# Performance work log

Measured on AMD Instinct MI355X. Metric: run time of the kernel, lower is better.

## Reference

```python
import jax, jax.numpy as jnp
import numpy as np

GROUPS = 32
EPS = 1e-6


def group_norm(x, gamma, beta):
    b, h, w, c = x.shape
    xg = x.reshape(b, h, w, GROUPS, c // GROUPS)
    mean = jnp.mean(xg, axis=(1, 2, 4), keepdims=True)
    var = jnp.var(xg, axis=(1, 2, 4), keepdims=True)
    xg = (xg - mean) * jax.lax.rsqrt(var + EPS)
    return xg.reshape(b, h, w, c) * gamma + beta


def setup_inputs() -> dict:
    key = jax.random.key(0)
    ks = jax.random.split(key, 6)
    B, H, W, C = 4, 64, 64, 512
    scale = 0.02
    return {
        "x": jax.random.normal(ks[0], (B, H, W, C), dtype=jnp.float32),
        "gamma": jnp.ones((C,), dtype=jnp.float32),
        "beta": jnp.zeros((C,), dtype=jnp.float32),
        "wq": jax.random.normal(ks[1], (C, C), dtype=jnp.float32) * scale,
        "bq": jnp.zeros((C,), dtype=jnp.float32),
        "wk": jax.random.normal(ks[2], (C, C), dtype=jnp.float32) * scale,
        "bk": jnp.zeros((C,), dtype=jnp.float32),
        "wv": jax.random.normal(ks[3], (C, C), dtype=jnp.float32) * scale,
        "bv": jnp.zeros((C,), dtype=jnp.float32),
        "wo": jax.random.normal(ks[4], (C, C), dtype=jnp.float32) * scale,
        "bo": jnp.zeros((C,), dtype=jnp.float32),
    }


def reference(x, gamma, beta, wq, bq, wk, bk, wv, bv, wo, bo):
    b, h, w, c = x.shape
    xn = group_norm(x, gamma, beta)
    # 1x1 convs == per-pixel linear layers
    q = (jnp.einsum('bhwc,cd->bhwd', xn, wq) + bq).reshape(b, h * w, c)
    k = (jnp.einsum('bhwc,cd->bhwd', xn, wk) + bk).reshape(b, h * w, c)
    v = (jnp.einsum('bhwc,cd->bhwd', xn, wv) + bv).reshape(b, h * w, c)
    # full (hw x hw) attention, single head
    scores = jnp.einsum('bic,bjc->bij', q, k) * (c ** -0.5)  # [b, hw, hw]
    attn = jax.nn.softmax(scores, axis=-1)
    out = jnp.einsum('bij,bjc->bic', attn, v).reshape(b, h, w, c)
    return jnp.einsum('bhwc,cd->bhwd', out, wo) + bo + x
```

## Files before the change

### kernel.cpp

```cpp
#include <hip/hip_runtime.h>
#include <stdint.h>


typedef __attribute__((ext_vector_type(8))) short bf16x8;
typedef __attribute__((ext_vector_type(8))) unsigned short u16x8;
typedef __attribute__((ext_vector_type(4))) float f32x4;

#define SOFTMAX_SCALE 0.044194173824159216f
#define QSCALE 0.06376237087058025f

__device__ __forceinline__ unsigned short f2bf(float f) {
  unsigned int x = __float_as_uint(f);
  x += 0x7fffu + ((x >> 16) & 1u);
  return (unsigned short)(x >> 16);
}
__device__ __forceinline__ float bf2f(unsigned short u) {
  return __uint_as_float((unsigned int)u << 16);
}

__device__ __forceinline__ void gl_lds16(const void* g, void* l) {
  __builtin_amdgcn_global_load_lds(
      (__attribute__((address_space(1))) unsigned char*)g,
      (__attribute__((address_space(3))) unsigned char*)l, 16, 0, 0);
}

__device__ __forceinline__ void gemm_tile(
    const unsigned short* __restrict__ A, long lda,
    const unsigned short* __restrict__ B, long ldb,
    int K, unsigned short* As, unsigned short* Bs, f32x4 acc[4][4]) {
  const int tid = threadIdx.x;
  const int wave = tid >> 6, lane = tid & 63;
  const int srow = lane >> 3;
  const int gg = lane & 7;
  const int wm = (wave >> 1) * 64, wn = (wave & 1) * 64;
  const int lrow = lane & 15;
  const int rsw = lrow & 7;
  const int kgb = lane >> 4;

  for (int k0 = 0; k0 < K; k0 += 64) {
    __syncthreads();
    for (int i = 0; i < 4; ++i) {
      int chunk = wave * 4 + i;
      int row = chunk * 8 + srow;
      int soffA = (gg ^ srow) * 16;
      int soffB = (gg ^ ((chunk * 2 + (srow >> 2)) & 7)) * 16;
      gl_lds16((const char*)(A + (long)row * lda + k0) + soffA, (char*)As + chunk * 1024);
      gl_lds16((const char*)(B + (long)row * ldb + k0) + soffB, (char*)Bs + chunk * 1024);
    }
    __syncthreads();
#pragma unroll
    for (int ks = 0; ks < 2; ++ks) {
      bf16x8 af[4], bfr[4];
      const int off = ((ks * 4 + kgb) ^ rsw) * 8;
#pragma unroll
      for (int t = 0; t < 4; ++t) {
        af[t]  = *(const bf16x8*)&As[(wm + t * 16 + lrow) * 64 + off];
        bfr[t] = *(const bf16x8*)&Bs[(wn + 4 * lrow + t) * 64 + off];
      }
#pragma unroll
      for (int mt = 0; mt < 4; ++mt)
#pragma unroll
        for (int nt = 0; nt < 4; ++nt)
          acc[mt][nt] = __builtin_amdgcn_mfma_f32_16x16x32_bf16(af[mt], bfr[nt], acc[mt][nt], 0, 0, 0);
    }
  }
}

#define EPILOG_SETUP                                          \
  const int lane = threadIdx.x & 63, wave = threadIdx.x >> 6; \
  const int wm = (wave >> 1) * 64, wn = (wave & 1) * 64;      \
  const int lcol4 = (lane & 15) * 4, lrb = (lane >> 4) * 4;

__global__ void prep_kernel(const float* __restrict__ wq, const float* __restrict__ wk,
                            const float* __restrict__ wv, const float* __restrict__ wo,
                            const float* __restrict__ bq, const float* __restrict__ bk,
                            const float* __restrict__ bv,
                            unsigned short* __restrict__ wqkvT,
                            unsigned short* __restrict__ woT,
                            float* __restrict__ bias, float* __restrict__ stats,
                            float* __restrict__ lsum) {
  long id = (long)blockIdx.x * 256 + threadIdx.x;
  if (id < 786432) {
    long n = id >> 9, k = id & 511;
    const float* w = (n < 512) ? wq : (n < 1024 ? wk : wv);
    wqkvT[id] = f2bf(w[k * 512 + (n & 511)]);
  } else if (id < 786432 + 262144) {
    long j = id - 786432, n = j >> 9, k = j & 511;
    woT[j] = f2bf(wo[k * 512 + n]);
  } else if (id < 786432 + 262144 + 1536) {
    long j = id - 786432 - 262144;
    bias[j] = (j < 512) ? bq[j] : (j < 1024 ? bk[j - 512] : bv[j - 1024]);
  } else if (id < 786432 + 262144 + 1536 + 256) {
    stats[id - 786432 - 262144 - 1536] = 0.f;
  } else if (id < 786432 + 262144 + 1536 + 256 + 16384) {
    lsum[id - 786432 - 262144 - 1536 - 256] = 0.f;
  }
}

__global__ __launch_bounds__(256) void gn_stats(const float* __restrict__ x,
                                                float* __restrict__ stats) {
  const int b = blockIdx.x >> 7, slab = blockIdx.x & 127;
  const float* xp = x + (long)b * 4096 * 512 + (long)slab * 32 * 512;
  const int tid = threadIdx.x;
  float s = 0.f, s2 = 0.f;
  for (int it = 0; it < 16; ++it) {
    int i = it * 256 + tid;
    float4 v = *(const float4*)(xp + (long)i * 4);
    s += v.x + v.y + v.z + v.w;
    s2 += v.x * v.x + v.y * v.y + v.z * v.z + v.w * v.w;
  }
  s += __shfl_xor(s, 1); s += __shfl_xor(s, 2);
  s2 += __shfl_xor(s2, 1); s2 += __shfl_xor(s2, 2);
  if ((tid & 3) == 0) {
    int g = (tid & 127) >> 2;
    atomicAdd(&stats[(b * 32 + g) * 2], s);
    atomicAdd(&stats[(b * 32 + g) * 2 + 1], s2);
  }
}

__global__ __launch_bounds__(256) void gn_apply(const float* __restrict__ x,
                                                const float* __restrict__ stats,
                                                const float* __restrict__ gamma,
                                                const float* __restrict__ beta,
                                                unsigned short* __restrict__ xn) {
  long id = (long)blockIdx.x * 256 + threadIdx.x;
  long a = id * 4;
  int b = (int)(id >> 19);
  int ch = (int)(a & 511);
  int g = ch >> 4;
  float s = stats[(b * 32 + g) * 2], s2 = stats[(b * 32 + g) * 2 + 1];
  float mean = s * (1.f / 65536.f);
  float rinv = rsqrtf(s2 * (1.f / 65536.f) - mean * mean + 1e-6f);
  float4 v = *(const float4*)(x + a);
  float4 gm = *(const float4*)(gamma + ch);
  float4 bt = *(const float4*)(beta + ch);
  ushort4 o;
  o.x = f2bf((v.x - mean) * rinv * gm.x + bt.x);
  o.y = f2bf((v.y - mean) * rinv * gm.y + bt.y);
  o.z = f2bf((v.z - mean) * rinv * gm.z + bt.z);
  o.w = f2bf((v.w - mean) * rinv * gm.w + bt.w);
  *(ushort4*)(xn + a) = o;
}

__global__ __launch_bounds__(256) void qkv_kernel(
    const unsigned short* __restrict__ xn, const unsigned short* __restrict__ wqkvT,
    const float* __restrict__ bias, unsigned short* __restrict__ q,
    unsigned short* __restrict__ kk, unsigned short* __restrict__ vv) {
  __shared__ unsigned short As[128 * 64], Bs[128 * 64];
  f32x4 acc[4][4] = {};
  const long tm = (long)blockIdx.x * 128, tn = (long)blockIdx.y * 128;
  gemm_tile(xn + tm * 512, 512, wqkvT + tn * 512, 512, 512, As, Bs, acc);
  EPILOG_SETUP
  const int region = (int)(tn >> 9);
  unsigned short* dst = region == 0 ? q : (region == 1 ? kk : vv);
  const long nloc = (tn & 511) + wn + lcol4;
  const float sc = region == 0 ? QSCALE : 1.f;
  float4 bs = *(const float4*)&bias[tn + wn + lcol4];
#pragma unroll
  for (int mt = 0; mt < 4; ++mt)
#pragma unroll
    for (int r = 0; r < 4; ++r) {
      long m = tm + wm + mt * 16 + lrb + r;
      ushort4 o;
      o.x = f2bf((acc[mt][0][r] + bs.x) * sc);
      o.y = f2bf((acc[mt][1][r] + bs.y) * sc);
      o.z = f2bf((acc[mt][2][r] + bs.z) * sc);
      o.w = f2bf((acc[mt][3][r] + bs.w) * sc);
      *(ushort4*)&dst[m * 512 + nloc] = o;
    }
}

__global__ __launch_bounds__(256) void transpose_v(const unsigned short* __restrict__ v,
                                                   unsigned short* __restrict__ vT) {
  const int b = blockIdx.z;
  const long j0 = (long)blockIdx.x * 64, c0 = (long)blockIdx.y * 64;
  __shared__ unsigned short t[64][72];
  const int tc = (threadIdx.x & 15) * 4, tr = threadIdx.x >> 4;
  for (int rr = 0; rr < 64; rr += 16) {
    ushort4 u = *(const ushort4*)&v[((long)b * 4096 + j0 + tr + rr) * 512 + c0 + tc];
    t[tr + rr][tc] = u.x; t[tr + rr][tc + 1] = u.y;
    t[tr + rr][tc + 2] = u.z; t[tr + rr][tc + 3] = u.w;
  }
  __syncthreads();
  for (int rr = 0; rr < 64; rr += 16) {
    int c = tr + rr;
    ushort4 o;
    o.x = t[tc + 0][c]; o.y = t[tc + 1][c]; o.z = t[tc + 2][c]; o.w = t[tc + 3][c];
    *(ushort4*)&vT[((long)b * 512 + c0 + c) * 4096 + j0 + tc] = o;
  }
}

__global__ __launch_bounds__(256) void qkt_kernel(
    const unsigned short* __restrict__ q, const unsigned short* __restrict__ kk,
    unsigned short* __restrict__ probs, float* __restrict__ lsum, int b0) {
  __shared__ unsigned short As[128 * 64], Bs[128 * 64];
  f32x4 acc[4][4] = {};
  const int z = blockIdx.z;
  const long bb = (long)(b0 + z) * 4096 * 512;
  const long tm = (long)blockIdx.x * 128, tn = (long)blockIdx.y * 128;
  gemm_tile(q + bb + tm * 512, 512, kk + bb + tn * 512, 512, 512, As, Bs, acc);
  EPILOG_SETUP
  unsigned short* out = probs + (long)z * 4096 * 4096;
  float* ls = lsum + (long)(b0 + z) * 4096;
  const long n0 = tn + wn + lcol4;
#pragma unroll
  for (int mt = 0; mt < 4; ++mt) {
    float rs[4];
#pragma unroll
    for (int r = 0; r < 4; ++r) {
      float e0 = exp2f(acc[mt][0][r]);
      float e1 = exp2f(acc[mt][1][r]);
      float e2 = exp2f(acc[mt][2][r]);
      float e3 = exp2f(acc[mt][3][r]);
      rs[r] = (e0 + e1) + (e2 + e3);
      ushort4 o;
      o.x = f2bf(e0); o.y = f2bf(e1); o.z = f2bf(e2); o.w = f2bf(e3);
      long m = tm + wm + mt * 16 + lrb + r;
      *(ushort4*)&out[m * 4096 + n0] = o;
    }
#pragma unroll
    for (int r = 0; r < 4; ++r) {
      float s = rs[r];
      s += __shfl_xor(s, 1); s += __shfl_xor(s, 2);
      s += __shfl_xor(s, 4); s += __shfl_xor(s, 8);
      if (lcol4 == 0) atomicAdd(&ls[tm + wm + mt * 16 + lrb + r], s);
    }
  }
}

__global__ __launch_bounds__(256) void pv_kernel(
    const unsigned short* __restrict__ probs, const unsigned short* __restrict__ vT,
    unsigned short* __restrict__ part, int b0) {
  __shared__ unsigned short As[128 * 64], Bs[128 * 64];
  f32x4 acc[4][4] = {};
  const int zb = blockIdx.z >> 1, s = blockIdx.z & 1;
  const long tm = (long)blockIdx.x * 128, tn = (long)blockIdx.y * 128;
  gemm_tile(probs + (long)zb * 4096 * 4096 + tm * 4096 + s * 2048, 4096,
            vT + (long)(b0 + zb) * 512 * 4096 + tn * 4096 + s * 2048, 4096,
            2048, As, Bs, acc);
  EPILOG_SETUP
  unsigned short* out = part + (long)blockIdx.z * 4096 * 512;
  const long n0 = tn + wn + lcol4;
#pragma unroll
  for (int mt = 0; mt < 4; ++mt)
#pragma unroll
    for (int r = 0; r < 4; ++r) {
      long m = tm + wm + mt * 16 + lrb + r;
      ushort4 o;
      o.x = f2bf(acc[mt][0][r]); o.y = f2bf(acc[mt][1][r]);
      o.z = f2bf(acc[mt][2][r]); o.w = f2bf(acc[mt][3][r]);
      *(ushort4*)&out[m * 512 + n0] = o;
    }
}

__global__ __launch_bounds__(256) void reduce_kernel(const unsigned short* __restrict__ part,
                                                     const float* __restrict__ lsum,
                                                     unsigned short* __restrict__ attn,
                                                     int b0) {
  const long elems = 4096l * 512;
  const int zb = blockIdx.y;
  const unsigned short* pp = part + (long)zb * 2 * elems;
  long id = (long)blockIdx.x * 256 + threadIdx.x;
  long a = id * 8;
  int m = (int)(a >> 9);
  float inv = 1.f / lsum[(long)(b0 + zb) * 4096 + m];
  u16x8 p0 = *(const u16x8*)(pp + a);
  u16x8 p1 = *(const u16x8*)(pp + elems + a);
  u16x8 o;
#pragma unroll
  for (int j = 0; j < 8; ++j)
    o[j] = f2bf((bf2f(p0[j]) + bf2f(p1[j])) * inv);
  *(u16x8*)(attn + (long)(b0 + zb) * elems + a) = o;
}

__global__ __launch_bounds__(256) void proj_kernel(
    const unsigned short* __restrict__ attn, const unsigned short* __restrict__ woT,
    const float* __restrict__ bo, const float* __restrict__ x,
    float* __restrict__ out) {
  __shared__ unsigned short As[128 * 64], Bs[128 * 64];
  f32x4 acc[4][4] = {};
  const long tm = (long)blockIdx.x * 128, tn = (long)blockIdx.y * 128;
  gemm_tile(attn + tm * 512, 512, woT + tn * 512, 512, 512, As, Bs, acc);
  EPILOG_SETUP
  const long n0 = tn + wn + lcol4;
  float4 bs = *(const float4*)&bo[n0];
#pragma unroll
  for (int mt = 0; mt < 4; ++mt)
#pragma unroll
    for (int r = 0; r < 4; ++r) {
      long m = tm + wm + mt * 16 + lrb + r;
      float4 xv = *(const float4*)&x[m * 512 + n0];
      float4 o;
      o.x = acc[mt][0][r] + bs.x + xv.x;
      o.y = acc[mt][1][r] + bs.y + xv.y;
      o.z = acc[mt][2][r] + bs.z + xv.z;
      o.w = acc[mt][3][r] + bs.w + xv.w;
      *(float4*)&((float*)out)[m * 512 + n0] = o;
    }
}

extern "C" void kernel_launch(void* const* d_in, const int* in_sizes, int n_in,
                              void* d_out, int out_size, void* d_ws, size_t ws_size,
                              hipStream_t stream) {
  const float* x     = (const float*)d_in[0];
  const float* gamma = (const float*)d_in[1];
  const float* beta  = (const float*)d_in[2];
  const float* wq    = (const float*)d_in[3];
  const float* bq    = (const float*)d_in[4];
  const float* wk    = (const float*)d_in[5];
  const float* bk    = (const float*)d_in[6];
  const float* wv    = (const float*)d_in[7];
  const float* bv    = (const float*)d_in[8];
  const float* wo    = (const float*)d_in[9];
  const float* bo    = (const float*)d_in[10];

  char* p = (char*)d_ws;
  auto take = [&](size_t bytes) { char* r = p; p += (bytes + 255) & ~(size_t)255; return r; };
  const long NTOK = 16384, C = 512, HW = 4096;
  unsigned short* xn    = (unsigned short*)take(NTOK * C * 2);
  unsigned short* q     = (unsigned short*)take(NTOK * C * 2);
  unsigned short* kbuf  = (unsigned short*)take(NTOK * C * 2);
  unsigned short* vT    = (unsigned short*)take(NTOK * C * 2);
  unsigned short* wqkvT = (unsigned short*)take(1536l * 512 * 2);
  unsigned short* woT   = (unsigned short*)take(512l * 512 * 2);
  float* bias           = (float*)take(1536 * 4);
  float* stats          = (float*)take(256 * 4);
  float* lsum           = (float*)take(16384 * 4);

  size_t fixed = (size_t)(p - (char*)d_ws);
  size_t per_nb = (size_t)HW * HW * 2 + 2ul * HW * C * 2 + 512;
  int NB = (ws_size >= fixed + 4 * per_nb) ? 4
         : (ws_size >= fixed + 2 * per_nb) ? 2 : 1;
  unsigned short* probs = (unsigned short*)take((size_t)NB * HW * HW * 2);
  unsigned short* part  = (unsigned short*)take((size_t)NB * 2 * HW * C * 2);
  unsigned short* attn  = xn;
  unsigned short* vbuf  = probs;

  prep_kernel<<<4168, 256, 0, stream>>>(wq, wk, wv, wo, bq, bk, bv, wqkvT, woT,
                                        bias, stats, lsum);
  gn_stats<<<512, 256, 0, stream>>>(x, stats);
  gn_apply<<<8192, 256, 0, stream>>>(x, stats, gamma, beta, xn);

  qkv_kernel<<<dim3(128, 12), 256, 0, stream>>>(xn, wqkvT, bias, q, kbuf, vbuf);
  transpose_v<<<dim3(64, 8, 4), 256, 0, stream>>>(vbuf, vT);

  for (int b0 = 0; b0 < 4; b0 += NB) {
    qkt_kernel<<<dim3(32, 32, NB), 256, 0, stream>>>(q, kbuf, probs, lsum, b0);
    pv_kernel<<<dim3(32, 4, 2 * NB), 256, 0, stream>>>(probs, vT, part, b0);
    reduce_kernel<<<dim3(1024, NB), 256, 0, stream>>>(part, lsum, attn, b0);
  }

  proj_kernel<<<dim3(128, 4), 256, 0, stream>>>(attn, woT, bo, x, (float*)d_out);
}
```

Before: 401.1 us.

## Double-buffer LDS in GEMM tiles and fuse split-K reduce into PV epilogue

Rewrites the shared GEMM tile loop to ping-pong between two LDS buffers so global-to-LDS loads of the next K slice overlap MFMA compute on the current one, halving barriers per slice. The PV kernel no longer splits K in two; it runs the full 4096-long reduction and applies the softmax normalization in its epilogue, removing the separate reduce kernel and the partial buffer round-trip. This doubles LDS per block, which may lower occupancy, and halves the PV grid size.

```diff
diff --git a/kernel.cpp b/kernel.cpp
--- a/kernel.cpp
+++ b/kernel.cpp
@@ -27,7 +27,10 @@
 __device__ __forceinline__ void gemm_tile(
     const unsigned short* __restrict__ A, long lda,
     const unsigned short* __restrict__ B, long ldb,
-    int K, unsigned short* As, unsigned short* Bs, f32x4 acc[4][4]) {
+    int K,
+    unsigned short* As0, unsigned short* As1,
+    unsigned short* Bs0, unsigned short* Bs1,
+    f32x4 acc[4][4]) {
   const int tid = threadIdx.x;
   const int wave = tid >> 6, lane = tid & 63;
   const int srow = lane >> 3;
@@ -37,25 +40,27 @@
   const int rsw = lrow & 7;
   const int kgb = lane >> 4;
 
-  for (int k0 = 0; k0 < K; k0 += 64) {
-    __syncthreads();
+  auto STAGE = [&](unsigned short* as, unsigned short* bs, int k0) {
+#pragma unroll
     for (int i = 0; i < 4; ++i) {
       int chunk = wave * 4 + i;
       int row = chunk * 8 + srow;
       int soffA = (gg ^ srow) * 16;
       int soffB = (gg ^ ((chunk * 2 + (srow >> 2)) & 7)) * 16;
-      gl_lds16((const char*)(A + (long)row * lda + k0) + soffA, (char*)As + chunk * 1024);
-      gl_lds16((const char*)(B + (long)row * ldb + k0) + soffB, (char*)Bs + chunk * 1024);
-    }
-    __syncthreads();
+      gl_lds16((const char*)(A + (long)row * lda + k0) + soffA, (char*)as + chunk * 1024);
+      gl_lds16((const char*)(B + (long)row * ldb + k0) + soffB, (char*)bs + chunk * 1024);
+    }
+  };
+
+  auto COMPUTE = [&](const unsigned short* as, const unsigned short* bs) {
 #pragma unroll
     for (int ks = 0; ks < 2; ++ks) {
       bf16x8 af[4], bfr[4];
       const int off = ((ks * 4 + kgb) ^ rsw) * 8;
 #pragma unroll
       for (int t = 0; t < 4; ++t) {
-        af[t]  = *(const bf16x8*)&As[(wm + t * 16 + lrow) * 64 + off];
-        bfr[t] = *(const bf16x8*)&Bs[(wn + 4 * lrow + t) * 64 + off];
+        af[t]  = *(const bf16x8*)&as[(wm + t * 16 + lrow) * 64 + off];
+        bfr[t] = *(const bf16x8*)&bs[(wn + 4 * lrow + t) * 64 + off];
       }
 #pragma unroll
       for (int mt = 0; mt < 4; ++mt)
@@ -63,8 +68,24 @@
         for (int nt = 0; nt < 4; ++nt)
           acc[mt][nt] = __builtin_amdgcn_mfma_f32_16x16x32_bf16(af[mt], bfr[nt], acc[mt][nt], 0, 0, 0);
     }
-  }
-}
+  };
+
+  const int nk = K >> 6;
+  STAGE(As0, Bs0, 0);
+  __syncthreads();
+  for (int t = 0; t < nk; t += 2) {
+    if (t + 1 < nk) STAGE(As1, Bs1, (t + 1) * 64);
+    COMPUTE(As0, Bs0);
+    __syncthreads();
+    if (t + 2 < nk) STAGE(As0, Bs0, (t + 2) * 64);
+    COMPUTE(As1, Bs1);
+    __syncthreads();
+  }
+}
+
+#define GEMM_SHARED                                              \
+  __shared__ unsigned short As0[128 * 64], As1[128 * 64];        \
+  __shared__ unsigned short Bs0[128 * 64], Bs1[128 * 64];
 
 #define EPILOG_SETUP                                          \
   const int lane = threadIdx.x & 63, wave = threadIdx.x >> 6; \
@@ -146,10 +167,10 @@
     const unsigned short* __restrict__ xn, const unsigned short* __restrict__ wqkvT,
     const float* __restrict__ bias, unsigned short* __restrict__ q,
     unsigned short* __restrict__ kk, unsigned short* __restrict__ vv) {
-  __shared__ unsigned short As[128 * 64], Bs[128 * 64];
+  GEMM_SHARED
   f32x4 acc[4][4] = {};
   const long tm = (long)blockIdx.x * 128, tn = (long)blockIdx.y * 128;
-  gemm_tile(xn + tm * 512, 512, wqkvT + tn * 512, 512, 512, As, Bs, acc);
+  gemm_tile(xn + tm * 512, 512, wqkvT + tn * 512, 512, 512, As0, As1, Bs0, Bs1, acc);
   EPILOG_SETUP
   const int region = (int)(tn >> 9);
   unsigned short* dst = region == 0 ? q : (region == 1 ? kk : vv);
@@ -193,12 +214,12 @@
 __global__ __launch_bounds__(256) void qkt_kernel(
     const unsigned short* __restrict__ q, const unsigned short* __restrict__ kk,
     unsigned short* __restrict__ probs, float* __restrict__ lsum, int b0) {
-  __shared__ unsigned short As[128 * 64], Bs[128 * 64];
+  GEMM_SHARED
   f32x4 acc[4][4] = {};
   const int z = blockIdx.z;
   const long bb = (long)(b0 + z) * 4096 * 512;
   const long tm = (long)blockIdx.x * 128, tn = (long)blockIdx.y * 128;
-  gemm_tile(q + bb + tm * 512, 512, kk + bb + tn * 512, 512, 512, As, Bs, acc);
+  gemm_tile(q + bb + tm * 512, 512, kk + bb + tn * 512, 512, 512, As0, As1, Bs0, Bs1, acc);
   EPILOG_SETUP
   unsigned short* out = probs + (long)z * 4096 * 4096;
   float* ls = lsum + (long)(b0 + z) * 4096;
@@ -230,57 +251,39 @@
 
 __global__ __launch_bounds__(256) void pv_kernel(
     const unsigned short* __restrict__ probs, const unsigned short* __restrict__ vT,
-    unsigned short* __restrict__ part, int b0) {
-  __shared__ unsigned short As[128 * 64], Bs[128 * 64];
+    const float* __restrict__ lsum, unsigned short* __restrict__ attn, int b0) {
+  GEMM_SHARED
   f32x4 acc[4][4] = {};
-  const int zb = blockIdx.z >> 1, s = blockIdx.z & 1;
+  const int z = blockIdx.z;
   const long tm = (long)blockIdx.x * 128, tn = (long)blockIdx.y * 128;
-  gemm_tile(probs + (long)zb * 4096 * 4096 + tm * 4096 + s * 2048, 4096,
-            vT + (long)(b0 + zb) * 512 * 4096 + tn * 4096 + s * 2048, 4096,
-            2048, As, Bs, acc);
+  gemm_tile(probs + (long)z * 4096 * 4096 + tm * 4096, 4096,
+            vT + (long)(b0 + z) * 512 * 4096 + tn * 4096, 4096,
+            4096, As0, As1, Bs0, Bs1, acc);
   EPILOG_SETUP
-  unsigned short* out = part + (long)blockIdx.z * 4096 * 512;
+  unsigned short* out = attn + (long)(b0 + z) * 4096 * 512;
+  const float* ls = lsum + (long)(b0 + z) * 4096;
   const long n0 = tn + wn + lcol4;
 #pragma unroll
   for (int mt = 0; mt < 4; ++mt)
 #pragma unroll
     for (int r = 0; r < 4; ++r) {
       long m = tm + wm + mt * 16 + lrb + r;
+      float inv = __builtin_amdgcn_rcpf(ls[m]);
       ushort4 o;
-      o.x = f2bf(acc[mt][0][r]); o.y = f2bf(acc[mt][1][r]);
-      o.z = f2bf(acc[mt][2][r]); o.w = f2bf(acc[mt][3][r]);
+      o.x = f2bf(acc[mt][0][r] * inv); o.y = f2bf(acc[mt][1][r] * inv);
+      o.z = f2bf(acc[mt][2][r] * inv); o.w = f2bf(acc[mt][3][r] * inv);
       *(ushort4*)&out[m * 512 + n0] = o;
     }
-}
-
-__global__ __launch_bounds__(256) void reduce_kernel(const unsigned short* __restrict__ part,
-                                                     const float* __restrict__ lsum,
-                                                     unsigned short* __restrict__ attn,
-                                                     int b0) {
-  const long elems = 4096l * 512;
-  const int zb = blockIdx.y;
-  const unsigned short* pp = part + (long)zb * 2 * elems;
-  long id = (long)blockIdx.x * 256 + threadIdx.x;
-  long a = id * 8;
-  int m = (int)(a >> 9);
-  float inv = 1.f / lsum[(long)(b0 + zb) * 4096 + m];
-  u16x8 p0 = *(const u16x8*)(pp + a);
-  u16x8 p1 = *(const u16x8*)(pp + elems + a);
-  u16x8 o;
-#pragma unroll
-  for (int j = 0; j < 8; ++j)
-    o[j] = f2bf((bf2f(p0[j]) + bf2f(p1[j])) * inv);
-  *(u16x8*)(attn + (long)(b0 + zb) * elems + a) = o;
 }
 
 __global__ __launch_bounds__(256) void proj_kernel(
     const unsigned short* __restrict__ attn, const unsigned short* __restrict__ woT,
     const float* __restrict__ bo, const float* __restrict__ x,
     float* __restrict__ out) {
-  __shared__ unsigned short As[128 * 64], Bs[128 * 64];
+  GEMM_SHARED
   f32x4 acc[4][4] = {};
   const long tm = (long)blockIdx.x * 128, tn = (long)blockIdx.y * 128;
-  gemm_tile(attn + tm * 512, 512, woT + tn * 512, 512, 512, As, Bs, acc);
+  gemm_tile(attn + tm * 512, 512, woT + tn * 512, 512, 512, As0, As1, Bs0, Bs1, acc);
   EPILOG_SETUP
   const long n0 = tn + wn + lcol4;
   float4 bs = *(const float4*)&bo[n0];
@@ -328,11 +331,10 @@
   float* lsum           = (float*)take(16384 * 4);
 
   size_t fixed = (size_t)(p - (char*)d_ws);
-  size_t per_nb = (size_t)HW * HW * 2 + 2ul * HW * C * 2 + 512;
+  size_t per_nb = (size_t)HW * HW * 2 + 512;
   int NB = (ws_size >= fixed + 4 * per_nb) ? 4
          : (ws_size >= fixed + 2 * per_nb) ? 2 : 1;
   unsigned short* probs = (unsigned short*)take((size_t)NB * HW * HW * 2);
-  unsigned short* part  = (unsigned short*)take((size_t)NB * 2 * HW * C * 2);
   unsigned short* attn  = xn;
   unsigned short* vbuf  = probs;
 
@@ -346,8 +348,7 @@
 
   for (int b0 = 0; b0 < 4; b0 += NB) {
     qkt_kernel<<<dim3(32, 32, NB), 256, 0, stream>>>(q, kbuf, probs, lsum, b0);
-    pv_kernel<<<dim3(32, 4, 2 * NB), 256, 0, stream>>>(probs, vT, part, b0);
-    reduce_kernel<<<dim3(1024, NB), 256, 0, stream>>>(part, lsum, attn, b0);
+    pv_kernel<<<dim3(32, 4, NB), 256, 0, stream>>>(probs, vT, lsum, attn, b0);
   }
 
   proj_kernel<<<dim3(128, 4), 256, 0, stream>>>(attn, woT, bo, x, (float*)d_out);
```

After: 367.5 us. -8.4%, faster.

## Double-buffer LDS in shared GEMM tile and add XCD-aware block remap for QK^T

Applied to the files above, without the earlier changes.

The shared GEMM tile now uses two LDS buffers, so the global-to-LDS load for the next K step is issued while MFMAs run on the current one, with one barrier per step instead of two. The QK^T kernel remaps block indices so each XCD works on a contiguous group of Q and K tiles, aiming for better L2 reuse. The PV kernel keeps a single-buffer variant with a simpler B swizzle and scalar stores, so its output tile layout changes. This doubles LDS per block, which may lower occupancy, and the PV path now writes 2-byte scalars instead of vector stores.

```diff
diff --git a/kernel.cpp b/kernel.cpp
--- a/kernel.cpp
+++ b/kernel.cpp
@@ -6,7 +6,6 @@
 typedef __attribute__((ext_vector_type(8))) unsigned short u16x8;
 typedef __attribute__((ext_vector_type(4))) float f32x4;
 
-#define SOFTMAX_SCALE 0.044194173824159216f
 #define QSCALE 0.06376237087058025f
 
 __device__ __forceinline__ unsigned short f2bf(float f) {
@@ -27,7 +26,10 @@
 __device__ __forceinline__ void gemm_tile(
     const unsigned short* __restrict__ A, long lda,
     const unsigned short* __restrict__ B, long ldb,
-    int K, unsigned short* As, unsigned short* Bs, f32x4 acc[4][4]) {
+    int K,
+    unsigned short* As0, unsigned short* As1,
+    unsigned short* Bs0, unsigned short* Bs1,
+    f32x4 acc[4][4]) {
   const int tid = threadIdx.x;
   const int wave = tid >> 6, lane = tid & 63;
   const int srow = lane >> 3;
@@ -37,15 +39,78 @@
   const int rsw = lrow & 7;
   const int kgb = lane >> 4;
 
+  auto STAGE = [&](unsigned short* as, unsigned short* bs, int k0) {
+#pragma unroll
+    for (int i = 0; i < 4; ++i) {
+      int chunk = wave * 4 + i;
+      int row = chunk * 8 + srow;
+      int soffA = (gg ^ srow) * 16;
+      int soffB = (gg ^ ((chunk * 2 + (srow >> 2)) & 7)) * 16;
+      gl_lds16((const char*)(A + (long)row * lda + k0) + soffA, (char*)as + chunk * 1024);
+      gl_lds16((const char*)(B + (long)row * ldb + k0) + soffB, (char*)bs + chunk * 1024);
+    }
+  };
+
+  auto COMPUTE = [&](const unsigned short* as, const unsigned short* bs) {
+#pragma unroll
+    for (int ks = 0; ks < 2; ++ks) {
+      bf16x8 af[4], bfr[4];
+      const int off = ((ks * 4 + kgb) ^ rsw) * 8;
+#pragma unroll
+      for (int t = 0; t < 4; ++t) {
+        af[t]  = *(const bf16x8*)&as[(wm + t * 16 + lrow) * 64 + off];
+        bfr[t] = *(const bf16x8*)&bs[(wn + 4 * lrow + t) * 64 + off];
+      }
+#pragma unroll
+      for (int mt = 0; mt < 4; ++mt)
+#pragma unroll
+        for (int nt = 0; nt < 4; ++nt)
+          acc[mt][nt] = __builtin_amdgcn_mfma_f32_16x16x32_bf16(af[mt], bfr[nt], acc[mt][nt], 0, 0, 0);
+    }
+  };
+
+  const int nk = K >> 6;
+  STAGE(As0, Bs0, 0);
+  __syncthreads();
+  for (int t = 0; t < nk; t += 2) {
+    if (t + 1 < nk) STAGE(As1, Bs1, (t + 1) * 64);
+    COMPUTE(As0, Bs0);
+    __syncthreads();
+    if (t + 2 < nk) STAGE(As0, Bs0, (t + 2) * 64);
+    COMPUTE(As1, Bs1);
+    __syncthreads();
+  }
+}
+
+#define GEMM_SHARED                                              \
+  __shared__ unsigned short As0[128 * 64], As1[128 * 64];        \
+  __shared__ unsigned short Bs0[128 * 64], Bs1[128 * 64];
+
+#define EPILOG_SETUP                                          \
+  const int lane = threadIdx.x & 63, wave = threadIdx.x >> 6; \
+  const int wm = (wave >> 1) * 64, wn = (wave & 1) * 64;      \
+  const int lcol4 = (lane & 15) * 4, lrb = (lane >> 4) * 4;
+
+__device__ __forceinline__ void gemm_tile_sb(
+    const unsigned short* __restrict__ A, long lda,
+    const unsigned short* __restrict__ B, long ldb,
+    int K, unsigned short* As, unsigned short* Bs, f32x4 acc[4][4]) {
+  const int tid = threadIdx.x;
+  const int wave = tid >> 6, lane = tid & 63;
+  const int srow = lane >> 3;
+  const int soff = ((lane & 7) ^ srow) * 16;
+  const int wm = (wave >> 1) * 64, wn = (wave & 1) * 64;
+  const int lrow = lane & 15;
+  const int rsw = lrow & 7;
+  const int kgb = lane >> 4;
+
   for (int k0 = 0; k0 < K; k0 += 64) {
     __syncthreads();
     for (int i = 0; i < 4; ++i) {
       int chunk = wave * 4 + i;
       int row = chunk * 8 + srow;
-      int soffA = (gg ^ srow) * 16;
-      int soffB = (gg ^ ((chunk * 2 + (srow >> 2)) & 7)) * 16;
-      gl_lds16((const char*)(A + (long)row * lda + k0) + soffA, (char*)As + chunk * 1024);
-      gl_lds16((const char*)(B + (long)row * ldb + k0) + soffB, (char*)Bs + chunk * 1024);
+      gl_lds16((const char*)(A + (long)row * lda + k0) + soff, (char*)As + chunk * 1024);
+      gl_lds16((const char*)(B + (long)row * ldb + k0) + soff, (char*)Bs + chunk * 1024);
     }
     __syncthreads();
 #pragma unroll
@@ -55,7 +120,7 @@
 #pragma unroll
       for (int t = 0; t < 4; ++t) {
         af[t]  = *(const bf16x8*)&As[(wm + t * 16 + lrow) * 64 + off];
-        bfr[t] = *(const bf16x8*)&Bs[(wn + 4 * lrow + t) * 64 + off];
+        bfr[t] = *(const bf16x8*)&Bs[(wn + t * 16 + lrow) * 64 + off];
       }
 #pragma unroll
       for (int mt = 0; mt < 4; ++mt)
@@ -65,11 +130,6 @@
     }
   }
 }
-
-#define EPILOG_SETUP                                          \
-  const int lane = threadIdx.x & 63, wave = threadIdx.x >> 6; \
-  const int wm = (wave >> 1) * 64, wn = (wave & 1) * 64;      \
-  const int lcol4 = (lane & 15) * 4, lrb = (lane >> 4) * 4;
 
 __global__ void prep_kernel(const float* __restrict__ wq, const float* __restrict__ wk,
                             const float* __restrict__ wv, const float* __restrict__ wo,
@@ -146,10 +206,10 @@
     const unsigned short* __restrict__ xn, const unsigned short* __restrict__ wqkvT,
     const float* __restrict__ bias, unsigned short* __restrict__ q,
     unsigned short* __restrict__ kk, unsigned short* __restrict__ vv) {
-  __shared__ unsigned short As[128 * 64], Bs[128 * 64];
+  GEMM_SHARED
   f32x4 acc[4][4] = {};
   const long tm = (long)blockIdx.x * 128, tn = (long)blockIdx.y * 128;
-  gemm_tile(xn + tm * 512, 512, wqkvT + tn * 512, 512, 512, As, Bs, acc);
+  gemm_tile(xn + tm * 512, 512, wqkvT + tn * 512, 512, 512, As0, As1, Bs0, Bs1, acc);
   EPILOG_SETUP
   const int region = (int)(tn >> 9);
   unsigned short* dst = region == 0 ? q : (region == 1 ? kk : vv);
@@ -193,12 +253,16 @@
 __global__ __launch_bounds__(256) void qkt_kernel(
     const unsigned short* __restrict__ q, const unsigned short* __restrict__ kk,
     unsigned short* __restrict__ probs, float* __restrict__ lsum, int b0) {
-  __shared__ unsigned short As[128 * 64], Bs[128 * 64];
+  GEMM_SHARED
   f32x4 acc[4][4] = {};
   const int z = blockIdx.z;
   const long bb = (long)(b0 + z) * 4096 * 512;
-  const long tm = (long)blockIdx.x * 128, tn = (long)blockIdx.y * 128;
-  gemm_tile(q + bb + tm * 512, 512, kk + bb + tn * 512, 512, 512, As, Bs, acc);
+  const int lin = (int)(blockIdx.x + 32 * blockIdx.y);
+  const int xcd = lin & 7, idx = lin >> 3;
+  const int tmi = (xcd & 3) * 8 + (idx & 7);
+  const int tni = (xcd >> 2) * 16 + (idx >> 3);
+  const long tm = (long)tmi * 128, tn = (long)tni * 128;
+  gemm_tile(q + bb + tm * 512, 512, kk + bb + tn * 512, 512, 512, As0, As1, Bs0, Bs1, acc);
   EPILOG_SETUP
   unsigned short* out = probs + (long)z * 4096 * 4096;
   float* ls = lsum + (long)(b0 + z) * 4096;
@@ -235,22 +299,23 @@
   f32x4 acc[4][4] = {};
   const int zb = blockIdx.z >> 1, s = blockIdx.z & 1;
   const long tm = (long)blockIdx.x * 128, tn = (long)blockIdx.y * 128;
-  gemm_tile(probs + (long)zb * 4096 * 4096 + tm * 4096 + s * 2048, 4096,
-            vT + (long)(b0 + zb) * 512 * 4096 + tn * 4096 + s * 2048, 4096,
-            2048, As, Bs, acc);
-  EPILOG_SETUP
+  gemm_tile_sb(probs + (long)zb * 4096 * 4096 + tm * 4096 + s * 2048, 4096,
+               vT + (long)(b0 + zb) * 512 * 4096 + tn * 4096 + s * 2048, 4096,
+               2048, As, Bs, acc);
+  const int lane = threadIdx.x & 63, wave = threadIdx.x >> 6;
+  const int wm = (wave >> 1) * 64, wn = (wave & 1) * 64;
+  const int lcol = lane & 15, lrb = (lane >> 4) * 4;
   unsigned short* out = part + (long)blockIdx.z * 4096 * 512;
-  const long n0 = tn + wn + lcol4;
 #pragma unroll
   for (int mt = 0; mt < 4; ++mt)
 #pragma unroll
-    for (int r = 0; r < 4; ++r) {
-      long m = tm + wm + mt * 16 + lrb + r;
-      ushort4 o;
-      o.x = f2bf(acc[mt][0][r]); o.y = f2bf(acc[mt][1][r]);
-      o.z = f2bf(acc[mt][2][r]); o.w = f2bf(acc[mt][3][r]);
-      *(ushort4*)&out[m * 512 + n0] = o;
-    }
+    for (int nt = 0; nt < 4; ++nt)
+#pragma unroll
+      for (int r = 0; r < 4; ++r) {
+        long m = tm + wm + mt * 16 + lrb + r;
+        long n = tn + wn + nt * 16 + lcol;
+        out[m * 512 + n] = f2bf(acc[mt][nt][r]);
+      }
 }
 
 __global__ __launch_bounds__(256) void reduce_kernel(const unsigned short* __restrict__ part,
@@ -277,10 +342,10 @@
     const unsigned short* __restrict__ attn, const unsigned short* __restrict__ woT,
     const float* __restrict__ bo, const float* __restrict__ x,
     float* __restrict__ out) {
-  __shared__ unsigned short As[128 * 64], Bs[128 * 64];
+  GEMM_SHARED
   f32x4 acc[4][4] = {};
   const long tm = (long)blockIdx.x * 128, tn = (long)blockIdx.y * 128;
-  gemm_tile(attn + tm * 512, 512, woT + tn * 512, 512, 512, As, Bs, acc);
+  gemm_tile(attn + tm * 512, 512, woT + tn * 512, 512, 512, As0, As1, Bs0, Bs1, acc);
   EPILOG_SETUP
   const long n0 = tn + wn + lcol4;
   float4 bs = *(const float4*)&bo[n0];
```

Result: faster. 381.6 us (-4.9%).
